# Performance work log

Measured on AMD Instinct MI355X. Metric: run time of the kernel, lower is better.

## Reference

```python
import jax, jax.numpy as jnp
import numpy as np

N = 100000       # nodes
DEG = 16         # fixed out/in degree used to build CSR
E = N * DEG      # edges
D_IN = 128       # in_feats
D_OUT = 256      # out_feats
K = 32           # maxk k_value


def _xavier_uniform(key, shape, gain):
    fan_out, fan_in = shape
    bound = gain * np.sqrt(6.0 / (fan_in + fan_out))
    return jax.random.uniform(key, shape, jnp.float32, -bound, bound)


def setup_inputs() -> dict:
    key = jax.random.key(0)
    ks = jax.random.split(key, 6)
    feat = jax.random.normal(ks[0], (N, D_IN), jnp.float32)
    topk_values = jax.random.uniform(ks[1], (N, K), jnp.float32)
    topk_indices = jax.random.randint(ks[2], (N, K), 0, D_IN).astype(jnp.int32)
    # CSR graph: fixed degree -> indptr is arange*DEG; random destinations
    indptr = (jnp.arange(N + 1) * DEG).astype(jnp.int32)
    indices = jax.random.randint(ks[3], (E,), 0, N).astype(jnp.int32)
    # set_graph_data: csr weight[e] = 1 / clamp(in_degree(dst), 1)
    in_deg = jax.ops.segment_sum(jnp.ones(E, jnp.float32), indices, num_segments=N)
    in_deg = jnp.maximum(in_deg, 1.0)
    csr_values = 1.0 / in_deg[indices]
    gain = np.sqrt(2.0)  # calculate_gain('relu')
    w_neigh = _xavier_uniform(ks[4], (D_OUT, D_IN), gain)
    w_self = _xavier_uniform(ks[5], (D_OUT, D_IN), gain)
    b_self = jnp.zeros((D_OUT,), jnp.float32)
    return {"feat": feat, "topk_values": topk_values, "csr_values": csr_values,
            "w_neigh": w_neigh, "w_self": w_self, "b_self": b_self,
            "topk_indices": topk_indices, "indptr": indptr, "indices": indices}


def reference(feat, topk_values, csr_values, w_neigh, w_self, b_self,
              topk_indices, indptr, indices):
    # Densify the k-sparse MaxK features: x[n, topk_indices[n, j]] = topk_values[n, j]
    x = jnp.zeros((N, D_IN), feat.dtype).at[
        jnp.arange(N)[:, None], topk_indices].add(topk_values)
    # Edge-weight-normalized SpMM over CSR: out[row] += w[e] * x[col[e]]
    row_ids = jnp.repeat(jnp.arange(N), jnp.diff(indptr), total_repeat_length=E)
    msgs = x[indices] * csr_values[:, None]          # [E, D_IN]
    agg = jax.ops.segment_sum(msgs, row_ids, num_segments=N)  # [N, D_IN]
    # lin_before_mp is False (in_feats <= out_feats): project after aggregation
    h_neigh = agg @ w_neigh.T                        # [N, D_OUT]
    rst = feat @ w_self.T + b_self + h_neigh         # fc_self(h_self) + h_neigh
    return rst
```

## Files before the change

### kernel.cpp

```cpp
#include <hip/hip_runtime.h>
#include <hip/hip_bf16.h>
#include <stdint.h>

#define N_NODES 100000
#define DEG 16
#define D_IN 128
#define D_OUT 256
#define K_TOP 32
#define K_CAT 256

typedef __attribute__((ext_vector_type(8))) short short8;
typedef __attribute__((ext_vector_type(4))) float floatx4;

__device__ __forceinline__ unsigned pack_bf16_rne(float f) {
    union { float f; unsigned u; } c; c.f = f;
    unsigned u = c.u;
    return (u + 0x7fffu + ((u >> 16) & 1u)) >> 16;
}
__device__ __forceinline__ float bf16lo_to_f(unsigned lo16) {
    union { unsigned u; float f; } c; c.u = lo16 << 16; return c.f;
}

typedef __attribute__((address_space(1))) void as1_void;
typedef __attribute__((address_space(3))) void as3_void;
__device__ __forceinline__ void gload_lds16(const void* g, void* l) {
    __builtin_amdgcn_global_load_lds((as1_void*)g, (as3_void*)l, 16, 0, 0);
}

#define DB 1563
#define DROWS 64
__global__ __launch_bounds__(256) void k_prep(const float* __restrict__ topk_v,
                                              const int* __restrict__ topk_i,
                                              const float* __restrict__ feat,
                                              const float* __restrict__ w_self,
                                              const float* __restrict__ w_neigh,
                                              unsigned short* __restrict__ xbf,
                                              unsigned short* __restrict__ fbf,
                                              unsigned short* __restrict__ bmat) {
    __shared__ float sx[DROWS * D_IN];
    const int t = threadIdx.x;
    if (blockIdx.x >= DB) {
        const int o = blockIdx.x - DB;
        float v = (t < D_IN) ? w_self[o * D_IN + t] : w_neigh[o * D_IN + (t - D_IN)];
        bmat[o * K_CAT + t] = (unsigned short)pack_bf16_rne(v);
        return;
    }
    const int row0 = blockIdx.x * DROWS;

    #pragma unroll
    for (int p = 0; p < 8; ++p)
        *(floatx4*)&sx[(t + p * 256) * 4] = (floatx4){0.f, 0.f, 0.f, 0.f};
    __syncthreads();

    const size_t tbase = (size_t)row0 * K_TOP;
    #pragma unroll
    for (int p = 0; p < 8; ++p) {
        int q = t + p * 256;
        int r = q >> 5;
        if (row0 + r < N_NODES) {
            int   ci = topk_i[tbase + q];
            float cv = topk_v[tbase + q];
            atomicAdd(&sx[r * D_IN + ci], cv);
        }
    }
    __syncthreads();

    #pragma unroll
    for (int p = 0; p < 16; ++p) {
        int d = t + p * 256;
        int r = d >> 6;
        int c2 = (d & 63) * 2;
        if (row0 + r < N_NODES) {
            float2 v = *(const float2*)&sx[r * D_IN + c2];
            ((unsigned*)(xbf + (size_t)(row0 + r) * D_IN))[d & 63] =
                pack_bf16_rne(v.x) | (pack_bf16_rne(v.y) << 16);
        }
    }

    #pragma unroll
    for (int p = 0; p < 8; ++p) {
        int q = t + p * 256;
        int r = q >> 5;
        int c4 = (q & 31) * 4;
        if (row0 + r < N_NODES) {
            float4 f = *(const float4*)(feat + (size_t)(row0 + r) * D_IN + c4);
            uint2 pk;
            pk.x = pack_bf16_rne(f.x) | (pack_bf16_rne(f.y) << 16);
            pk.y = pack_bf16_rne(f.z) | (pack_bf16_rne(f.w) << 16);
            ((uint2*)(fbf + (size_t)(row0 + r) * D_IN))[q & 31] = pk;
        }
    }
}

#define BM 128
#define BN 256
#define BK 32
#define NTA 4
#define NT  8

__global__ __launch_bounds__(512, 2) void k_fused(const float* __restrict__ csr_w,
                                                  const int* __restrict__ col_idx,
                                                  const unsigned short* __restrict__ xbf,
                                                  const unsigned short* __restrict__ fbf,
                                                  const unsigned short* __restrict__ bmat,
                                                  const float* __restrict__ bias,
                                                  float* __restrict__ out) {
    __shared__ __align__(16) unsigned short Agg[BM * 128];
    __shared__ __align__(16) unsigned short As[2][BM * BK];
    const int t    = threadIdx.x;
    const int lane = t & 63, wave = t >> 6;
    const int l16  = lane & 15, quad = lane >> 4;
    const int row0 = blockIdx.x * BM;

    const int a_r = wave * 16 + (lane >> 2);
    const int a_c = (lane & 3) * 8;
    int a_gr = row0 + a_r; if (a_gr >= N_NODES) a_gr = N_NODES - 1;
    const unsigned short* gA = fbf + (size_t)a_gr * D_IN + a_c;

#define STAGE_A(buf, tt) gload_lds16(gA + (tt) * BK, &As[buf][wave * 16 * BK])

    STAGE_A(0, 0);

    const int ql = lane & 15, qb = lane & 48;
    const int qrow = wave * 4 + (lane >> 4);

    int cc[4]; float ww[4];
    #pragma unroll
    for (int p = 0; p < 4; ++p) {
        const int gr = row0 + p * 32 + qrow;
        cc[p] = 0; ww[p] = 0.f;
        if (gr < N_NODES) {
            cc[p] = __builtin_nontemporal_load(col_idx + (size_t)gr * DEG + ql);
            ww[p] = __builtin_nontemporal_load(csr_w   + (size_t)gr * DEG + ql);
        }
    }

    uint4 vva[8], vvb[8];
    #pragma unroll
    for (int e = 0; e < 8; ++e) {
        int col = __shfl(cc[0], qb | e);
        vva[e] = *(const uint4*)(xbf + (size_t)col * D_IN + ql * 8);
    }
    float a[8] = {0.f, 0.f, 0.f, 0.f, 0.f, 0.f, 0.f, 0.f};

    #pragma unroll
    for (int s = 0; s < 8; ++s) {
        const int p  = s >> 1;
        const int e0 = (s & 1) * 8;
        if (s < 7) {
            const int np  = (s + 1) >> 1;
            const int ne0 = ((s + 1) & 1) * 8;
            #pragma unroll
            for (int e = 0; e < 8; ++e) {
                int col = __shfl(cc[np], qb | (ne0 + e));
                if (s & 1) vva[e] = *(const uint4*)(xbf + (size_t)col * D_IN + ql * 8);
                else       vvb[e] = *(const uint4*)(xbf + (size_t)col * D_IN + ql * 8);
            }
        }
        #pragma unroll
        for (int e = 0; e < 8; ++e) {
            float we = __shfl(ww[p], qb | (e0 + e));
            uint4 v = (s & 1) ? vvb[e] : vva[e];
            a[0] += we * bf16lo_to_f(v.x & 0xffffu);
            a[1] += we * bf16lo_to_f(v.x >> 16);
            a[2] += we * bf16lo_to_f(v.y & 0xffffu);
            a[3] += we * bf16lo_to_f(v.y >> 16);
            a[4] += we * bf16lo_to_f(v.z & 0xffffu);
            a[5] += we * bf16lo_to_f(v.z >> 16);
            a[6] += we * bf16lo_to_f(v.w & 0xffffu);
            a[7] += we * bf16lo_to_f(v.w >> 16);
        }
        if (s & 1) {
            const int r = p * 32 + qrow;
            uint4 pk;
            pk.x = pack_bf16_rne(a[0]) | (pack_bf16_rne(a[1]) << 16);
            pk.y = pack_bf16_rne(a[2]) | (pack_bf16_rne(a[3]) << 16);
            pk.z = pack_bf16_rne(a[4]) | (pack_bf16_rne(a[5]) << 16);
            pk.w = pack_bf16_rne(a[6]) | (pack_bf16_rne(a[7]) << 16);
            *(uint4*)&Agg[r * 128 + ((ql * 8) ^ ((r & 7) << 3))] = pk;
            #pragma unroll
            for (int z = 0; z < 8; ++z) a[z] = 0.f;
        }
    }

    const int wr = wave >> 2, wc = wave & 3;
    const unsigned short* gBw = bmat + (size_t)(wc * 64 + l16) * K_CAT + quad * 8;
    floatx4 acc[4][4];
    #pragma unroll
    for (int i = 0; i < 4; ++i)
        #pragma unroll
        for (int j = 0; j < 4; ++j)
            acc[i][j] = (floatx4){0.f, 0.f, 0.f, 0.f};

    __syncthreads();

    #pragma unroll
    for (int tt = 0; tt < NT; ++tt) {
        const int cur = tt & 1;
        if (tt + 1 < NTA) STAGE_A(cur ^ 1, tt + 1);

        short8 afr[4], bfr[4];
        #pragma unroll
        for (int j = 0; j < 4; ++j)
            bfr[j] = *(const short8*)(gBw + (size_t)j * 16 * K_CAT + tt * BK);
        if (tt < NTA) {
            #pragma unroll
            for (int i = 0; i < 4; ++i)
                afr[i] = *(const short8*)&As[cur][(wr * 64 + i * 16 + l16) * BK + quad * 8];
        } else {
            const int c0 = (tt - NTA) * 32 + quad * 8;
            #pragma unroll
            for (int i = 0; i < 4; ++i) {
                const int m = wr * 64 + i * 16 + l16;
                afr[i] = *(const short8*)&Agg[m * 128 + (c0 ^ ((m & 7) << 3))];
            }
        }

        #pragma unroll
        for (int i = 0; i < 4; ++i)
            #pragma unroll
            for (int j = 0; j < 4; ++j)
                acc[i][j] = __builtin_amdgcn_mfma_f32_16x16x32_bf16(bfr[j], afr[i], acc[i][j], 0, 0, 0);

        if (tt + 1 < NTA) __syncthreads();
    }

    #pragma unroll
    for (int j = 0; j < 4; ++j) {
        const int cg = wc * 64 + j * 16 + quad * 4;
        const floatx4 bv = *(const floatx4*)&bias[cg];
        #pragma unroll
        for (int i = 0; i < 4; ++i) {
            const int gr = row0 + wr * 64 + i * 16 + l16;
            if (gr < N_NODES) {
                floatx4 v = acc[i][j] + bv;
                __builtin_nontemporal_store(v, (floatx4*)(out + (size_t)gr * D_OUT + cg));
            }
        }
    }
#undef STAGE_A
}

extern "C" void kernel_launch(void* const* d_in, const int* in_sizes, int n_in,
                              void* d_out, int out_size, void* d_ws, size_t ws_size,
                              hipStream_t stream) {
    const float* feat    = (const float*)d_in[0];
    const float* topk_v  = (const float*)d_in[1];
    const float* csr_w   = (const float*)d_in[2];
    const float* w_neigh = (const float*)d_in[3];
    const float* w_self  = (const float*)d_in[4];
    const float* b_self  = (const float*)d_in[5];
    const int*   topk_i  = (const int*)d_in[6];
    const int*   indices = (const int*)d_in[8];
    float* out = (float*)d_out;

    unsigned short* xbf  = (unsigned short*)d_ws;
    unsigned short* fbf  = xbf + (size_t)N_NODES * D_IN;
    unsigned short* bmat = fbf + (size_t)N_NODES * D_IN;

    k_prep<<<dim3(DB + 256), dim3(256), 0, stream>>>(
        topk_v, topk_i, feat, w_self, w_neigh, xbf, fbf, bmat);
    k_fused<<<dim3((N_NODES + BM - 1) / BM), dim3(512), 0, stream>>>(
        csr_w, indices, xbf, fbf, bmat, b_self, out);
}
```

Measured before the change: 292.9 us.

## Double block to 1024 threads and stage weight tiles through LDS

The fused gather+GEMM kernel now runs 16 waves per 128-row tile instead of 8. Each wave gathers fewer neighbor rows and computes a 32x64 output sub-tile. The weight matrix B is now staged into a double-buffered LDS tile by waves 8-15, instead of every wave reading it directly from global memory. This aims to add memory-level parallelism for the random gathers and to cut redundant global B reads. In exchange it adds more LDS use, barriers on every K step, and fewer MFMAs per wave. The launch_bounds(1024,8) value looks unrealistic for the LDS footprint.

```diff
diff --git a/kernel.cpp b/kernel.cpp
--- a/kernel.cpp
+++ b/kernel.cpp
@@ -98,36 +98,44 @@
 #define NTA 4
 #define NT  8
 
-__global__ __launch_bounds__(512, 2) void k_fused(const float* __restrict__ csr_w,
-                                                  const int* __restrict__ col_idx,
-                                                  const unsigned short* __restrict__ xbf,
-                                                  const unsigned short* __restrict__ fbf,
-                                                  const unsigned short* __restrict__ bmat,
-                                                  const float* __restrict__ bias,
-                                                  float* __restrict__ out) {
+__global__ __launch_bounds__(1024, 8) void k_fused(const float* __restrict__ csr_w,
+                                                   const int* __restrict__ col_idx,
+                                                   const unsigned short* __restrict__ xbf,
+                                                   const unsigned short* __restrict__ fbf,
+                                                   const unsigned short* __restrict__ bmat,
+                                                   const float* __restrict__ bias,
+                                                   float* __restrict__ out) {
     __shared__ __align__(16) unsigned short Agg[BM * 128];
     __shared__ __align__(16) unsigned short As[2][BM * BK];
+    __shared__ __align__(16) unsigned short Bs[2][BN * BK];
     const int t    = threadIdx.x;
     const int lane = t & 63, wave = t >> 6;
     const int l16  = lane & 15, quad = lane >> 4;
     const int row0 = blockIdx.x * BM;
 
-    const int a_r = wave * 16 + (lane >> 2);
-    const int a_c = (lane & 3) * 8;
-    int a_gr = row0 + a_r; if (a_gr >= N_NODES) a_gr = N_NODES - 1;
-    const unsigned short* gA = fbf + (size_t)a_gr * D_IN + a_c;
-
-#define STAGE_A(buf, tt) gload_lds16(gA + (tt) * BK, &As[buf][wave * 16 * BK])
-
-    STAGE_A(0, 0);
+    const int s_r = (wave & 7) * 16 + (lane >> 2);
+    const int s_c = (lane & 3) * 8;
+    int a_gr = row0 + s_r; if (a_gr >= N_NODES) a_gr = N_NODES - 1;
+    const unsigned short* gA  = fbf  + (size_t)a_gr * D_IN + s_c;
+    const int b_r = (wave & 7) * 32 + (lane >> 2);
+    const unsigned short* gB0 = bmat + (size_t)b_r        * K_CAT + s_c;
+    const unsigned short* gB1 = bmat + (size_t)(b_r + 16) * K_CAT + s_c;
+
+#define STAGE_A(buf, tt) gload_lds16(gA + (tt) * BK, &As[buf][((wave & 7) * 16) * BK])
+#define STAGE_B(buf, tt) do {                                                   \
+        gload_lds16(gB0 + (tt) * BK, &Bs[buf][((wave & 7) * 32)      * BK]);    \
+        gload_lds16(gB1 + (tt) * BK, &Bs[buf][((wave & 7) * 32 + 16) * BK]);    \
+    } while (0)
+
+    if (wave < 8) STAGE_A(0, 0); else STAGE_B(0, 0);
 
     const int ql = lane & 15, qb = lane & 48;
     const int qrow = wave * 4 + (lane >> 4);
 
-    int cc[4]; float ww[4];
-    #pragma unroll
-    for (int p = 0; p < 4; ++p) {
-        const int gr = row0 + p * 32 + qrow;
+    int cc[2]; float ww[2];
+    #pragma unroll
+    for (int p = 0; p < 2; ++p) {
+        const int gr = row0 + p * 64 + qrow;
         cc[p] = 0; ww[p] = 0.f;
         if (gr < N_NODES) {
             cc[p] = __builtin_nontemporal_load(col_idx + (size_t)gr * DEG + ql);
@@ -135,9 +143,9 @@
         }
     }
 
-    uint4 vva[8], vvb[8];
-    #pragma unroll
-    for (int e = 0; e < 8; ++e) {
+    uint4 vva[4], vvb[4];
+    #pragma unroll
+    for (int e = 0; e < 4; ++e) {
         int col = __shfl(cc[0], qb | e);
         vva[e] = *(const uint4*)(xbf + (size_t)col * D_IN + ql * 8);
     }
@@ -145,20 +153,20 @@
 
     #pragma unroll
     for (int s = 0; s < 8; ++s) {
-        const int p  = s >> 1;
-        const int e0 = (s & 1) * 8;
+        const int p  = s >> 2;
+        const int e0 = (s & 3) * 4;
         if (s < 7) {
-            const int np  = (s + 1) >> 1;
-            const int ne0 = ((s + 1) & 1) * 8;
-            #pragma unroll
-            for (int e = 0; e < 8; ++e) {
+            const int np  = (s + 1) >> 2;
+            const int ne0 = ((s + 1) & 3) * 4;
+            #pragma unroll
+            for (int e = 0; e < 4; ++e) {
                 int col = __shfl(cc[np], qb | (ne0 + e));
                 if (s & 1) vva[e] = *(const uint4*)(xbf + (size_t)col * D_IN + ql * 8);
                 else       vvb[e] = *(const uint4*)(xbf + (size_t)col * D_IN + ql * 8);
             }
         }
         #pragma unroll
-        for (int e = 0; e < 8; ++e) {
+        for (int e = 0; e < 4; ++e) {
             float we = __shfl(ww[p], qb | (e0 + e));
             uint4 v = (s & 1) ? vvb[e] : vva[e];
             a[0] += we * bf16lo_to_f(v.x & 0xffffu);
@@ -170,8 +178,8 @@
             a[6] += we * bf16lo_to_f(v.w & 0xffffu);
             a[7] += we * bf16lo_to_f(v.w >> 16);
         }
-        if (s & 1) {
-            const int r = p * 32 + qrow;
+        if ((s & 3) == 3) {
+            const int r = p * 64 + qrow;
             uint4 pk;
             pk.x = pack_bf16_rne(a[0]) | (pack_bf16_rne(a[1]) << 16);
             pk.y = pack_bf16_rne(a[2]) | (pack_bf16_rne(a[3]) << 16);
@@ -184,10 +192,9 @@
     }
 
     const int wr = wave >> 2, wc = wave & 3;
-    const unsigned short* gBw = bmat + (size_t)(wc * 64 + l16) * K_CAT + quad * 8;
-    floatx4 acc[4][4];
-    #pragma unroll
-    for (int i = 0; i < 4; ++i)
+    floatx4 acc[2][4];
+    #pragma unroll
+    for (int i = 0; i < 2; ++i)
         #pragma unroll
         for (int j = 0; j < 4; ++j)
             acc[i][j] = (floatx4){0.f, 0.f, 0.f, 0.f};
@@ -197,32 +204,33 @@
     #pragma unroll
     for (int tt = 0; tt < NT; ++tt) {
         const int cur = tt & 1;
-        if (tt + 1 < NTA) STAGE_A(cur ^ 1, tt + 1);
-
-        short8 afr[4], bfr[4];
-        #pragma unroll
-        for (int j = 0; j < 4; ++j)
-            bfr[j] = *(const short8*)(gBw + (size_t)j * 16 * K_CAT + tt * BK);
+        if (wave < 8) { if (tt + 1 < NTA) STAGE_A(cur ^ 1, tt + 1); }
+        else          { if (tt + 1 < NT)  STAGE_B(cur ^ 1, tt + 1); }
+
+        short8 afr[2], bfr[4];
         if (tt < NTA) {
             #pragma unroll
-            for (int i = 0; i < 4; ++i)
-                afr[i] = *(const short8*)&As[cur][(wr * 64 + i * 16 + l16) * BK + quad * 8];
+            for (int i = 0; i < 2; ++i)
+                afr[i] = *(const short8*)&As[cur][(wr * 32 + i * 16 + l16) * BK + quad * 8];
         } else {
             const int c0 = (tt - NTA) * 32 + quad * 8;
             #pragma unroll
-            for (int i = 0; i < 4; ++i) {
-                const int m = wr * 64 + i * 16 + l16;
+            for (int i = 0; i < 2; ++i) {
+                const int m = wr * 32 + i * 16 + l16;
                 afr[i] = *(const short8*)&Agg[m * 128 + (c0 ^ ((m & 7) << 3))];
             }
         }
-
-        #pragma unroll
-        for (int i = 0; i < 4; ++i)
+        #pragma unroll
+        for (int j = 0; j < 4; ++j)
+            bfr[j] = *(const short8*)&Bs[cur][(wc * 64 + j * 16 + l16) * BK + quad * 8];
+
+        #pragma unroll
+        for (int i = 0; i < 2; ++i)
             #pragma unroll
             for (int j = 0; j < 4; ++j)
                 acc[i][j] = __builtin_amdgcn_mfma_f32_16x16x32_bf16(bfr[j], afr[i], acc[i][j], 0, 0, 0);
 
-        if (tt + 1 < NTA) __syncthreads();
+        if (tt + 1 < NT) __syncthreads();
     }
 
     #pragma unroll
@@ -230,8 +238,8 @@
         const int cg = wc * 64 + j * 16 + quad * 4;
         const floatx4 bv = *(const floatx4*)&bias[cg];
         #pragma unroll
-        for (int i = 0; i < 4; ++i) {
-            const int gr = row0 + wr * 64 + i * 16 + l16;
+        for (int i = 0; i < 2; ++i) {
+            const int gr = row0 + wr * 32 + i * 16 + l16;
             if (gr < N_NODES) {
                 floatx4 v = acc[i][j] + bv;
                 __builtin_nontemporal_store(v, (floatx4*)(out + (size_t)gr * D_OUT + cg));
@@ -239,6 +247,7 @@
         }
     }
 #undef STAGE_A
+#undef STAGE_B
 }
 
 extern "C" void kernel_launch(void* const* d_in, const int* in_sizes, int n_in,
@@ -260,6 +269,6 @@
 
     k_prep<<<dim3(DB + 256), dim3(256), 0, stream>>>(
         topk_v, topk_i, feat, w_self, w_neigh, xbf, fbf, bmat);
-    k_fused<<<dim3((N_NODES + BM - 1) / BM), dim3(512), 0, stream>>>(
+    k_fused<<<dim3((N_NODES + BM - 1) / BM), dim3(1024), 0, stream>>>(
         csr_w, indices, xbf, fbf, bmat, b_self, out);
 }
```

After: 295.0 us. About the same (+0.7%).
